# Kernel optimization log

Measured on AMD Instinct MI355X. Metric: run time of the kernel, lower is better.

The kernel has to match this reference:

```python
import jax, jax.numpy as jnp
import numpy as np

N = 50000
E = 1600000
IN_F = 256
OUT_F = 128
ALPHA = 0.2  # LeakyReLU negative slope


def setup_inputs() -> dict:
    key = jax.random.key(0)
    k1, k2, k3, k4, k5, k6 = jax.random.split(key, 6)
    h = jax.random.normal(k1, (N, IN_F), dtype=jnp.float32)
    src = jax.random.randint(k2, (E,), 0, N, dtype=jnp.int64)
    dst = jax.random.randint(k3, (E,), 0, N, dtype=jnp.int64)
    # xavier_uniform-style init
    def xavier(k, shape):
        bound = np.sqrt(6.0 / (shape[0] + shape[1]))
        return jax.random.uniform(k, shape, jnp.float32, -bound, bound)
    W = xavier(k4, (IN_F, OUT_F))
    a_src = xavier(k5, (OUT_F, 1))
    a_dst = xavier(k6, (OUT_F, 1))
    return {"h": h, "src": src, "dst": dst, "W": W, "a_src": a_src, "a_dst": a_dst}


def reference(h, src, dst, W, a_src, a_dst):
    n = h.shape[0]
    Wh = h @ W                                  # [N, OUT_F] dense GEMM
    f1 = (Wh @ a_src)[:, 0]                     # [N]
    f2 = (Wh @ a_dst)[:, 0]                     # [N]
    e = f1[src] + f2[dst]                       # [E] edge-wise gather
    e = jnp.where(e > 0, e, ALPHA * e)          # LeakyReLU
    # sparse softmax over each row (segment = src/row index)
    m = jax.ops.segment_max(e, src, num_segments=n)
    ex = jnp.exp(e - m[src])
    denom = jax.ops.segment_sum(ex, src, num_segments=n)
    att = ex / denom[src]                       # [E] normalized attention
    # sparse-dense matmul: h_prime[i] = sum_j att[ij] * Wh[j]
    h_prime = jax.ops.segment_sum(att[:, None] * Wh[dst], src, num_segments=n)
    return jax.nn.elu(h_prime)
```

## Files before the change

kernel.cpp:

```cpp
#include <hip/hip_runtime.h>
#include <hip/hip_bf16.h>
#include <math.h>

#define IN_F 256
#define OUT_F 128
#define ALPHA 0.2f

#define BSH 7
#define BNODES 128
#define CHUNK 8192
#define NBK 512
#define CAP 5120

typedef __attribute__((ext_vector_type(8))) short short8;
typedef __attribute__((ext_vector_type(4))) float f32x4;

static __device__ __forceinline__ unsigned short f2bf(float x) {
    union { __hip_bfloat16 h; unsigned short u; } cv;
    cv.h = __float2bfloat16(x);
    return cv.u;
}

static __device__ __forceinline__ float2 bf2u(unsigned int u) {
    union { float f; unsigned int i; } a, b;
    a.i = u << 16;
    b.i = u & 0xFFFF0000u;
    return make_float2(a.f, b.f);
}

__global__ __launch_bounds__(512) void scatter_gemm_kernel(
        const int* __restrict__ src, const int* __restrict__ dst,
        int* __restrict__ cursor, unsigned int* __restrict__ bin, int e, int nb,
        const float* __restrict__ h, const float* __restrict__ W,
        const float* __restrict__ a_src, const float* __restrict__ a_dst,
        unsigned short* __restrict__ Whb, float* __restrict__ f1,
        float* __restrict__ f2, int n, int nsc) {
    __shared__ union {
        struct {
            unsigned int ebuf[CHUNK];
            int lh[NBK];
            int ls[NBK];
            int ebase[NBK];
            int lx[NBK];
            int gbase[NBK];
        } sc;
        struct {
            unsigned short a[128 * 40];
            unsigned short b[128 * 40];
        } ge;
    } sm;
    int tid = threadIdx.x;

    if ((int)blockIdx.x < nsc) {
        int base = blockIdx.x * CHUNK;
        int count = e - base; if (count > CHUNK) count = CHUNK;

        for (int i = tid; i < nb; i += 512) sm.sc.lh[i] = 0;
        __syncthreads();
        for (int i = tid; i < count; i += 512) atomicAdd(&sm.sc.lh[src[base + i] >> BSH], 1);
        __syncthreads();
        int v = (tid < nb) ? sm.sc.lh[tid] : 0;
        sm.sc.ls[tid] = v;
        __syncthreads();
#pragma unroll
        for (int off = 1; off < NBK; off <<= 1) {
            int t = (tid >= off) ? sm.sc.ls[tid - off] : 0;
            __syncthreads();
            sm.sc.ls[tid] += t;
            __syncthreads();
        }
        if (tid < nb) {
            int ex = sm.sc.ls[tid] - v;
            sm.sc.ebase[tid] = ex;
            sm.sc.lx[tid] = ex;
        }
        __syncthreads();
        for (int i = tid; i < count; i += 512) {
            int s = src[base + i], d = dst[base + i];
            int b = s >> BSH;
            int p = atomicAdd(&sm.sc.lx[b], 1);
            sm.sc.ebuf[p] = ((unsigned int)(s & (BNODES - 1)) << 17) | (unsigned int)d;
        }
        __syncthreads();
        if (tid < nb) {
            int c = sm.sc.lh[tid];
            sm.sc.gbase[tid] = c ? atomicAdd(&cursor[tid], c) : 0;
        }
        __syncthreads();
        int wave = tid >> 6, lane = tid & 63;
        for (int b = wave; b < nb; b += 8) {
            int c = sm.sc.lh[b], eb = sm.sc.ebase[b], gb = sm.sc.gbase[b];
            size_t gb0 = (size_t)b * CAP + gb;
            for (int l = lane; l < c; l += 64) bin[gb0 + l] = sm.sc.ebuf[eb + l];
        }
    } else {
        int bid = blockIdx.x - nsc;
        int wv = tid >> 6, lane = tid & 63;
        int m = lane & 15, quad = lane >> 4;
        int r0 = bid * 128;

        f32x4 acc[8];
#pragma unroll
        for (int c = 0; c < 8; c++) acc[c] = (f32x4){0.f, 0.f, 0.f, 0.f};

        for (int k0 = 0; k0 < IN_F; k0 += 32) {
            {
                int arow = tid >> 3;
                int kq = tid & 7;
#pragma unroll
                for (int p = 0; p < 2; p++) {
                    int row = arow + p * 64;
                    int grow = r0 + row;
                    float4 v = make_float4(0.f, 0.f, 0.f, 0.f);
                    if (grow < n) v = *(const float4*)&h[(size_t)grow * IN_F + k0 + kq * 4];
                    ushort4 b;
                    b.x = f2bf(v.x); b.y = f2bf(v.y); b.z = f2bf(v.z); b.w = f2bf(v.w);
                    *(ushort4*)&sm.ge.a[row * 40 + kq * 4] = b;
                }
            }
            {
                int c4 = (tid & 31) * 4;
                int kb = tid >> 5;
#pragma unroll
                for (int p = 0; p < 2; p++) {
                    int kk = p * 16 + kb;
                    float4 wv4 = *(const float4*)&W[(size_t)(k0 + kk) * OUT_F + c4];
                    sm.ge.b[(c4 + 0) * 40 + kk] = f2bf(wv4.x);
                    sm.ge.b[(c4 + 1) * 40 + kk] = f2bf(wv4.y);
                    sm.ge.b[(c4 + 2) * 40 + kk] = f2bf(wv4.z);
                    sm.ge.b[(c4 + 3) * 40 + kk] = f2bf(wv4.w);
                }
            }
            __syncthreads();
            short8 af = *(const short8*)&sm.ge.a[(wv * 16 + m) * 40 + quad * 8];
#pragma unroll
            for (int c = 0; c < 8; c++) {
                short8 bfv = *(const short8*)&sm.ge.b[(c * 16 + m) * 40 + quad * 8];
                acc[c] = __builtin_amdgcn_mfma_f32_16x16x32_bf16(af, bfv, acc[c], 0, 0, 0);
            }
            __syncthreads();
        }

        int base_row = r0 + wv * 16 + quad * 4;
#pragma unroll
        for (int reg = 0; reg < 4; reg++) {
            int rg = base_row + reg;
            if (rg < n) {
#pragma unroll
                for (int c = 0; c < 8; c++)
                    Whb[(size_t)rg * OUT_F + c * 16 + m] = f2bf(acc[c][reg]);
            }
        }

        float a1[8], a2[8];
#pragma unroll
        for (int c = 0; c < 8; c++) {
            a1[c] = a_src[c * 16 + m];
            a2[c] = a_dst[c * 16 + m];
        }
        float p1[4] = {0.f, 0.f, 0.f, 0.f}, p2[4] = {0.f, 0.f, 0.f, 0.f};
#pragma unroll
        for (int c = 0; c < 8; c++)
#pragma unroll
            for (int reg = 0; reg < 4; reg++) {
                p1[reg] += acc[c][reg] * a1[c];
                p2[reg] += acc[c][reg] * a2[c];
            }
#pragma unroll
        for (int mask = 1; mask < 16; mask <<= 1)
#pragma unroll
            for (int reg = 0; reg < 4; reg++) {
                p1[reg] += __shfl_xor(p1[reg], mask, 64);
                p2[reg] += __shfl_xor(p2[reg], mask, 64);
            }
        if (m == 0) {
#pragma unroll
            for (int reg = 0; reg < 4; reg++) {
                int rg = base_row + reg;
                if (rg < n) { f1[rg] = p1[reg]; f2[rg] = p2[reg]; }
            }
        }
    }
}

__global__ __launch_bounds__(256) void sort_kernel(const int* __restrict__ cursor,
                                                   const unsigned int* __restrict__ bin,
                                                   uint2* __restrict__ edat,
                                                   int* __restrict__ offs,
                                                   int* __restrict__ deg,
                                                   const float* __restrict__ f1,
                                                   const float* __restrict__ f2, int n) {
    __shared__ unsigned int ebuf[CAP];
    __shared__ int lh[BNODES];
    __shared__ int lx[BNODES];
    __shared__ float lf1[BNODES];
    int b = blockIdx.x;
    int tid = threadIdx.x;
    int base = b * CAP;
    int K = cursor[b];
    if (K > CAP) K = CAP;
    for (int l = tid; l < BNODES; l += 256) {
        lh[l] = 0;
        int node = (b << BSH) + l;
        lf1[l] = (node < n) ? f1[node] : 0.f;
    }
    __syncthreads();
    for (int i = tid; i < K; i += 256) {
        unsigned int p = bin[base + i];
        ebuf[i] = p;
        atomicAdd(&lh[p >> 17], 1);
    }
    __syncthreads();
    int own = (tid < BNODES) ? lh[tid] : 0;
    for (int off = 1; off < BNODES; off <<= 1) {
        int v = (tid >= off && tid < BNODES) ? lh[tid - off] : 0;
        __syncthreads();
        if (tid < BNODES) lh[tid] += v;
        __syncthreads();
    }
    if (tid < BNODES) {
        int ex = lh[tid] - own;
        lx[tid] = ex;
        int node = (b << BSH) + tid;
        if (node < n) { offs[node] = base + ex; deg[node] = own; }
    }
    __syncthreads();
    for (int i = tid; i < K; i += 256) {
        unsigned int p = ebuf[i];
        int ls_ = p >> 17;
        int d = p & 0x1FFFF;
        int r = atomicAdd(&lx[ls_], 1);
        float e = lf1[ls_] + f2[d];
        e = e > 0.f ? e : ALPHA * e;
        edat[base + r] = make_uint2((unsigned int)d, __float_as_uint(__expf(e)));
    }
}

__global__ __launch_bounds__(256) void agg_kernel(const unsigned int* __restrict__ WhbU,
                                                  const int* __restrict__ offs,
                                                  const int* __restrict__ deg,
                                                  const uint2* __restrict__ edat,
                                                  float* __restrict__ out, int n) {
    int tid = threadIdx.x;
    int lane = tid & 63;
    int node = blockIdx.x * 4 + (tid >> 6);
    if (node >= n) return;
    int grp = lane >> 4;
    int c8 = lane & 15;
    int j0 = offs[node];
    int j1 = j0 + deg[node];
    float4 accA = make_float4(0.f, 0.f, 0.f, 0.f);
    float4 accB = make_float4(0.f, 0.f, 0.f, 0.f);
    float den = 0.f;

    int j = j0;
    int nmain = (j1 - j0) >> 4;
    if (nmain > 0) {
        uint2 e0 = edat[j + grp];
        uint2 e1 = edat[j + grp + 4];
        uint2 e2 = edat[j + grp + 8];
        uint2 e3 = edat[j + grp + 12];
        for (int it = 0; it < nmain; ++it) {
            uint4 w0 = *(const uint4*)&WhbU[(size_t)(e0.x << 6) + c8 * 4];
            uint4 w1 = *(const uint4*)&WhbU[(size_t)(e1.x << 6) + c8 * 4];
            uint4 w2 = *(const uint4*)&WhbU[(size_t)(e2.x << 6) + c8 * 4];
            uint4 w3 = *(const uint4*)&WhbU[(size_t)(e3.x << 6) + c8 * 4];
            float x0 = __uint_as_float(e0.y);
            float x1 = __uint_as_float(e1.y);
            float x2 = __uint_as_float(e2.y);
            float x3 = __uint_as_float(e3.y);
            int jn = j + 16;
            uint2 n0, n1, n2, n3;
            if (it + 1 < nmain) {
                n0 = edat[jn + grp];
                n1 = edat[jn + grp + 4];
                n2 = edat[jn + grp + 8];
                n3 = edat[jn + grp + 12];
            }
            float2 g;
            g = bf2u(w0.x); accA.x += x0 * g.x; accA.y += x0 * g.y;
            g = bf2u(w0.y); accA.z += x0 * g.x; accA.w += x0 * g.y;
            g = bf2u(w0.z); accB.x += x0 * g.x; accB.y += x0 * g.y;
            g = bf2u(w0.w); accB.z += x0 * g.x; accB.w += x0 * g.y;
            g = bf2u(w1.x); accA.x += x1 * g.x; accA.y += x1 * g.y;
            g = bf2u(w1.y); accA.z += x1 * g.x; accA.w += x1 * g.y;
            g = bf2u(w1.z); accB.x += x1 * g.x; accB.y += x1 * g.y;
            g = bf2u(w1.w); accB.z += x1 * g.x; accB.w += x1 * g.y;
            g = bf2u(w2.x); accA.x += x2 * g.x; accA.y += x2 * g.y;
            g = bf2u(w2.y); accA.z += x2 * g.x; accA.w += x2 * g.y;
            g = bf2u(w2.z); accB.x += x2 * g.x; accB.y += x2 * g.y;
            g = bf2u(w2.w); accB.z += x2 * g.x; accB.w += x2 * g.y;
            g = bf2u(w3.x); accA.x += x3 * g.x; accA.y += x3 * g.y;
            g = bf2u(w3.y); accA.z += x3 * g.x; accA.w += x3 * g.y;
            g = bf2u(w3.z); accB.x += x3 * g.x; accB.y += x3 * g.y;
            g = bf2u(w3.w); accB.z += x3 * g.x; accB.w += x3 * g.y;
            den += x0 + x1 + x2 + x3;
            j = jn;
            e0 = n0; e1 = n1; e2 = n2; e3 = n3;
        }
    }
    for (; j + 4 <= j1; j += 4) {
        uint2 e = edat[j + grp];
        uint4 w = *(const uint4*)&WhbU[(size_t)(e.x << 6) + c8 * 4];
        float x = __uint_as_float(e.y);
        float2 g;
        g = bf2u(w.x); accA.x += x * g.x; accA.y += x * g.y;
        g = bf2u(w.y); accA.z += x * g.x; accA.w += x * g.y;
        g = bf2u(w.z); accB.x += x * g.x; accB.y += x * g.y;
        g = bf2u(w.w); accB.z += x * g.x; accB.w += x * g.y;
        den += x;
    }
    if (j + grp < j1) {
        uint2 e = edat[j + grp];
        uint4 w = *(const uint4*)&WhbU[(size_t)(e.x << 6) + c8 * 4];
        float x = __uint_as_float(e.y);
        float2 g;
        g = bf2u(w.x); accA.x += x * g.x; accA.y += x * g.y;
        g = bf2u(w.y); accA.z += x * g.x; accA.w += x * g.y;
        g = bf2u(w.z); accB.x += x * g.x; accB.y += x * g.y;
        g = bf2u(w.w); accB.z += x * g.x; accB.w += x * g.y;
        den += x;
    }

#pragma unroll
    for (int mask = 16; mask < 64; mask <<= 1) {
        accA.x += __shfl_xor(accA.x, mask, 64);
        accA.y += __shfl_xor(accA.y, mask, 64);
        accA.z += __shfl_xor(accA.z, mask, 64);
        accA.w += __shfl_xor(accA.w, mask, 64);
        accB.x += __shfl_xor(accB.x, mask, 64);
        accB.y += __shfl_xor(accB.y, mask, 64);
        accB.z += __shfl_xor(accB.z, mask, 64);
        accB.w += __shfl_xor(accB.w, mask, 64);
        den += __shfl_xor(den, mask, 64);
    }

    if (grp == 0) {
        float inv = (j1 > j0) ? 1.f / den : 0.f;
        float r[8];
        r[0] = accA.x * inv; r[1] = accA.y * inv; r[2] = accA.z * inv; r[3] = accA.w * inv;
        r[4] = accB.x * inv; r[5] = accB.y * inv; r[6] = accB.z * inv; r[7] = accB.w * inv;
#pragma unroll
        for (int k = 0; k < 8; k++) r[k] = r[k] > 0.f ? r[k] : __expf(r[k]) - 1.f;
        float* op = &out[(size_t)node * OUT_F + c8 * 8];
        *(float4*)&op[0] = make_float4(r[0], r[1], r[2], r[3]);
        *(float4*)&op[4] = make_float4(r[4], r[5], r[6], r[7]);
    }
}

extern "C" void kernel_launch(void* const* d_in, const int* in_sizes, int n_in,
                              void* d_out, int out_size, void* d_ws, size_t ws_size,
                              hipStream_t stream) {
    const float* h     = (const float*)d_in[0];
    const int*   src   = (const int*)d_in[1];
    const int*   dst   = (const int*)d_in[2];
    const float* W     = (const float*)d_in[3];
    const float* a_src = (const float*)d_in[4];
    const float* a_dst = (const float*)d_in[5];
    float* out = (float*)d_out;

    const int N = in_sizes[0] / IN_F;
    const int E = in_sizes[1];
    const int NB = (N + BNODES - 1) >> BSH;
    const int NCH = (E + CHUNK - 1) / CHUNK;
    const int GB = (N + 127) / 128;

    char* ws = (char*)d_ws;
    size_t off = 0;
    auto alloc = [&](size_t bytes) -> void* {
        void* p = ws + off;
        off += (bytes + 255) & ~(size_t)255;
        return p;
    };
    unsigned short* Whb = (unsigned short*)alloc((size_t)N * OUT_F * 2);
    float* f1     = (float*)alloc((size_t)N * 4);
    float* f2     = (float*)alloc((size_t)N * 4);
    int*   cursor = (int*)alloc((size_t)NB * 4);
    int*   offs   = (int*)alloc((size_t)N * 4);
    int*   deg    = (int*)alloc((size_t)N * 4);
    unsigned int* bin  = (unsigned int*)alloc((size_t)NB * CAP * 4);
    uint2*        edat = (uint2*)alloc((size_t)NB * CAP * 8);
    (void)ws_size; (void)n_in; (void)out_size;

    hipMemsetAsync(cursor, 0, (size_t)NB * 4, stream);
    scatter_gemm_kernel<<<NCH + GB, 512, 0, stream>>>(src, dst, cursor, bin, E, NB,
                                                      h, W, a_src, a_dst, Whb, f1, f2, N, NCH);
    sort_kernel<<<NB, 256, 0, stream>>>(cursor, bin, edat, offs, deg, f1, f2, N);
    agg_kernel<<<(N + 3) / 4, 256, 0, stream>>>((const unsigned int*)Whb, offs, deg, edat, out, N);
}
```

Measured before the change: 211.6 us.

## Fuse bucket sort and aggregation into one kernel using LDS edge list

Merges the sort and aggregation kernels so each block sorts its 128-node bucket into shared memory and immediately aggregates from it. This drops the global edat/offs/deg round trip and one launch, and replaces the barrier-heavy LDS scan with a wave shuffle scan. The W tile load is also reorganized to pack 8 bf16 values per thread into one vector LDS store, and the accumulation uses packed float2 math. The trade-off is fewer blocks (one per 128 nodes, about 391) with large LDS use, which lowers occupancy and latency hiding for the gather-heavy aggregation. The explicit prefetch of the next edge group is also gone.

```diff
diff --git a/kernel.cpp b/kernel.cpp
--- a/kernel.cpp
+++ b/kernel.cpp
@@ -14,6 +14,7 @@
 
 typedef __attribute__((ext_vector_type(8))) short short8;
 typedef __attribute__((ext_vector_type(4))) float f32x4;
+typedef __attribute__((ext_vector_type(2))) float f32x2;
 
 static __device__ __forceinline__ unsigned short f2bf(float x) {
     union { __hip_bfloat16 h; unsigned short u; } cv;
@@ -21,11 +22,11 @@
     return cv.u;
 }
 
-static __device__ __forceinline__ float2 bf2u(unsigned int u) {
-    union { float f; unsigned int i; } a, b;
-    a.i = u << 16;
-    b.i = u & 0xFFFF0000u;
-    return make_float2(a.f, b.f);
+static __device__ __forceinline__ f32x2 up2(unsigned int u) {
+    union { float f; unsigned int i; } lo, hi;
+    lo.i = u << 16;
+    hi.i = u & 0xFFFF0000u;
+    return (f32x2){lo.f, hi.f};
 }
 
 __global__ __launch_bounds__(512) void scatter_gemm_kernel(
@@ -103,6 +104,9 @@
 #pragma unroll
         for (int c = 0; c < 8; c++) acc[c] = (f32x4){0.f, 0.f, 0.f, 0.f};
 
+        int bcol = tid & 127;
+        int bkq  = tid >> 7;
+
         for (int k0 = 0; k0 < IN_F; k0 += 32) {
             {
                 int arow = tid >> 3;
@@ -119,17 +123,14 @@
                 }
             }
             {
-                int c4 = (tid & 31) * 4;
-                int kb = tid >> 5;
-#pragma unroll
-                for (int p = 0; p < 2; p++) {
-                    int kk = p * 16 + kb;
-                    float4 wv4 = *(const float4*)&W[(size_t)(k0 + kk) * OUT_F + c4];
-                    sm.ge.b[(c4 + 0) * 40 + kk] = f2bf(wv4.x);
-                    sm.ge.b[(c4 + 1) * 40 + kk] = f2bf(wv4.y);
-                    sm.ge.b[(c4 + 2) * 40 + kk] = f2bf(wv4.z);
-                    sm.ge.b[(c4 + 3) * 40 + kk] = f2bf(wv4.w);
-                }
+                float vw[8];
+#pragma unroll
+                for (int j = 0; j < 8; ++j)
+                    vw[j] = W[(size_t)(k0 + bkq * 8 + j) * OUT_F + bcol];
+                union { short8 v; unsigned short u[8]; } pk;
+#pragma unroll
+                for (int j = 0; j < 8; ++j) pk.u[j] = f2bf(vw[j]);
+                *(short8*)&sm.ge.b[bcol * 40 + bkq * 8] = pk.v;
             }
             __syncthreads();
             short8 af = *(const short8*)&sm.ge.a[(wv * 16 + m) * 40 + quad * 8];
@@ -183,168 +184,150 @@
     }
 }
 
-__global__ __launch_bounds__(256) void sort_kernel(const int* __restrict__ cursor,
-                                                   const unsigned int* __restrict__ bin,
-                                                   uint2* __restrict__ edat,
-                                                   int* __restrict__ offs,
-                                                   int* __restrict__ deg,
-                                                   const float* __restrict__ f1,
-                                                   const float* __restrict__ f2, int n) {
-    __shared__ unsigned int ebuf[CAP];
+__global__ __launch_bounds__(512) void sortagg_kernel(
+        const int* __restrict__ cursor, const unsigned int* __restrict__ bin,
+        const float* __restrict__ f1, const float* __restrict__ f2,
+        const unsigned int* __restrict__ WhbU, float* __restrict__ out, int n) {
+    __shared__ uint2 eL[CAP];
     __shared__ int lh[BNODES];
-    __shared__ int lx[BNODES];
+    __shared__ int st[BNODES];
+    __shared__ int cur[BNODES];
+    __shared__ int scn[BNODES];
     __shared__ float lf1[BNODES];
     int b = blockIdx.x;
     int tid = threadIdx.x;
     int base = b * CAP;
     int K = cursor[b];
     if (K > CAP) K = CAP;
-    for (int l = tid; l < BNODES; l += 256) {
-        lh[l] = 0;
+
+    if (tid < BNODES) {
+        lh[tid] = 0;
+        int node = (b << BSH) + tid;
+        lf1[tid] = (node < n) ? f1[node] : 0.f;
+    }
+    __syncthreads();
+
+    unsigned int pe[10];
+#pragma unroll
+    for (int u = 0; u < 10; ++u) {
+        int i = tid + u * 512;
+        if (i < K) {
+            unsigned int p = bin[base + i];
+            pe[u] = p;
+            atomicAdd(&lh[p >> 17], 1);
+        }
+    }
+    __syncthreads();
+
+    if (tid < BNODES) {
+        int lane = tid & 63;
+        int s = lh[tid];
+#pragma unroll
+        for (int off = 1; off < 64; off <<= 1) {
+            int t = __shfl_up(s, off, 64);
+            if (lane >= off) s += t;
+        }
+        scn[tid] = s;
+    }
+    __syncthreads();
+    if (tid < BNODES) {
+        int inc = scn[tid] + ((tid >= 64) ? scn[63] : 0);
+        int start = inc - lh[tid];
+        st[tid] = start;
+        cur[tid] = start;
+    }
+    __syncthreads();
+
+#pragma unroll
+    for (int u = 0; u < 10; ++u) {
+        int i = tid + u * 512;
+        if (i < K) {
+            unsigned int p = pe[u];
+            int ls_ = p >> 17;
+            int d = p & 0x1FFFF;
+            int r = atomicAdd(&cur[ls_], 1);
+            float e = lf1[ls_] + f2[d];
+            e = e > 0.f ? e : ALPHA * e;
+            eL[r] = make_uint2((unsigned int)d, __float_as_uint(__expf(e)));
+        }
+    }
+    __syncthreads();
+
+    int wv = tid >> 6, lane = tid & 63;
+    int grp = lane >> 4, c8 = lane & 15;
+    for (int li = 0; li < 16; ++li) {
+        int l = (wv << 4) + li;
         int node = (b << BSH) + l;
-        lf1[l] = (node < n) ? f1[node] : 0.f;
-    }
-    __syncthreads();
-    for (int i = tid; i < K; i += 256) {
-        unsigned int p = bin[base + i];
-        ebuf[i] = p;
-        atomicAdd(&lh[p >> 17], 1);
-    }
-    __syncthreads();
-    int own = (tid < BNODES) ? lh[tid] : 0;
-    for (int off = 1; off < BNODES; off <<= 1) {
-        int v = (tid >= off && tid < BNODES) ? lh[tid - off] : 0;
-        __syncthreads();
-        if (tid < BNODES) lh[tid] += v;
-        __syncthreads();
-    }
-    if (tid < BNODES) {
-        int ex = lh[tid] - own;
-        lx[tid] = ex;
-        int node = (b << BSH) + tid;
-        if (node < n) { offs[node] = base + ex; deg[node] = own; }
-    }
-    __syncthreads();
-    for (int i = tid; i < K; i += 256) {
-        unsigned int p = ebuf[i];
-        int ls_ = p >> 17;
-        int d = p & 0x1FFFF;
-        int r = atomicAdd(&lx[ls_], 1);
-        float e = lf1[ls_] + f2[d];
-        e = e > 0.f ? e : ALPHA * e;
-        edat[base + r] = make_uint2((unsigned int)d, __float_as_uint(__expf(e)));
-    }
-}
-
-__global__ __launch_bounds__(256) void agg_kernel(const unsigned int* __restrict__ WhbU,
-                                                  const int* __restrict__ offs,
-                                                  const int* __restrict__ deg,
-                                                  const uint2* __restrict__ edat,
-                                                  float* __restrict__ out, int n) {
-    int tid = threadIdx.x;
-    int lane = tid & 63;
-    int node = blockIdx.x * 4 + (tid >> 6);
-    if (node >= n) return;
-    int grp = lane >> 4;
-    int c8 = lane & 15;
-    int j0 = offs[node];
-    int j1 = j0 + deg[node];
-    float4 accA = make_float4(0.f, 0.f, 0.f, 0.f);
-    float4 accB = make_float4(0.f, 0.f, 0.f, 0.f);
-    float den = 0.f;
-
-    int j = j0;
-    int nmain = (j1 - j0) >> 4;
-    if (nmain > 0) {
-        uint2 e0 = edat[j + grp];
-        uint2 e1 = edat[j + grp + 4];
-        uint2 e2 = edat[j + grp + 8];
-        uint2 e3 = edat[j + grp + 12];
-        for (int it = 0; it < nmain; ++it) {
-            uint4 w0 = *(const uint4*)&WhbU[(size_t)(e0.x << 6) + c8 * 4];
-            uint4 w1 = *(const uint4*)&WhbU[(size_t)(e1.x << 6) + c8 * 4];
-            uint4 w2 = *(const uint4*)&WhbU[(size_t)(e2.x << 6) + c8 * 4];
-            uint4 w3 = *(const uint4*)&WhbU[(size_t)(e3.x << 6) + c8 * 4];
+        int dg = lh[l];
+        int j = st[l];
+        int jend = j + dg;
+        f32x2 a0 = {0.f, 0.f}, a1 = {0.f, 0.f}, a2 = {0.f, 0.f}, a3 = {0.f, 0.f};
+        float den = 0.f;
+        for (; j + 16 <= jend; j += 16) {
+            uint2 e0 = eL[j + grp];
+            uint2 e1 = eL[j + grp + 4];
+            uint2 e2 = eL[j + grp + 8];
+            uint2 e3 = eL[j + grp + 12];
+            uint4 w0 = *(const uint4*)&WhbU[((size_t)e0.x << 6) + (c8 << 2)];
+            uint4 w1 = *(const uint4*)&WhbU[((size_t)e1.x << 6) + (c8 << 2)];
+            uint4 w2 = *(const uint4*)&WhbU[((size_t)e2.x << 6) + (c8 << 2)];
+            uint4 w3 = *(const uint4*)&WhbU[((size_t)e3.x << 6) + (c8 << 2)];
             float x0 = __uint_as_float(e0.y);
             float x1 = __uint_as_float(e1.y);
             float x2 = __uint_as_float(e2.y);
             float x3 = __uint_as_float(e3.y);
-            int jn = j + 16;
-            uint2 n0, n1, n2, n3;
-            if (it + 1 < nmain) {
-                n0 = edat[jn + grp];
-                n1 = edat[jn + grp + 4];
-                n2 = edat[jn + grp + 8];
-                n3 = edat[jn + grp + 12];
-            }
-            float2 g;
-            g = bf2u(w0.x); accA.x += x0 * g.x; accA.y += x0 * g.y;
-            g = bf2u(w0.y); accA.z += x0 * g.x; accA.w += x0 * g.y;
-            g = bf2u(w0.z); accB.x += x0 * g.x; accB.y += x0 * g.y;
-            g = bf2u(w0.w); accB.z += x0 * g.x; accB.w += x0 * g.y;
-            g = bf2u(w1.x); accA.x += x1 * g.x; accA.y += x1 * g.y;
-            g = bf2u(w1.y); accA.z += x1 * g.x; accA.w += x1 * g.y;
-            g = bf2u(w1.z); accB.x += x1 * g.x; accB.y += x1 * g.y;
-            g = bf2u(w1.w); accB.z += x1 * g.x; accB.w += x1 * g.y;
-            g = bf2u(w2.x); accA.x += x2 * g.x; accA.y += x2 * g.y;
-            g = bf2u(w2.y); accA.z += x2 * g.x; accA.w += x2 * g.y;
-            g = bf2u(w2.z); accB.x += x2 * g.x; accB.y += x2 * g.y;
-            g = bf2u(w2.w); accB.z += x2 * g.x; accB.w += x2 * g.y;
-            g = bf2u(w3.x); accA.x += x3 * g.x; accA.y += x3 * g.y;
-            g = bf2u(w3.y); accA.z += x3 * g.x; accA.w += x3 * g.y;
-            g = bf2u(w3.z); accB.x += x3 * g.x; accB.y += x3 * g.y;
-            g = bf2u(w3.w); accB.z += x3 * g.x; accB.w += x3 * g.y;
+            f32x2 xx;
+            xx = (f32x2){x0, x0};
+            a0 += xx * up2(w0.x); a1 += xx * up2(w0.y); a2 += xx * up2(w0.z); a3 += xx * up2(w0.w);
+            xx = (f32x2){x1, x1};
+            a0 += xx * up2(w1.x); a1 += xx * up2(w1.y); a2 += xx * up2(w1.z); a3 += xx * up2(w1.w);
+            xx = (f32x2){x2, x2};
+            a0 += xx * up2(w2.x); a1 += xx * up2(w2.y); a2 += xx * up2(w2.z); a3 += xx * up2(w2.w);
+            xx = (f32x2){x3, x3};
+            a0 += xx * up2(w3.x); a1 += xx * up2(w3.y); a2 += xx * up2(w3.z); a3 += xx * up2(w3.w);
             den += x0 + x1 + x2 + x3;
-            j = jn;
-            e0 = n0; e1 = n1; e2 = n2; e3 = n3;
-        }
-    }
-    for (; j + 4 <= j1; j += 4) {
-        uint2 e = edat[j + grp];
-        uint4 w = *(const uint4*)&WhbU[(size_t)(e.x << 6) + c8 * 4];
-        float x = __uint_as_float(e.y);
-        float2 g;
-        g = bf2u(w.x); accA.x += x * g.x; accA.y += x * g.y;
-        g = bf2u(w.y); accA.z += x * g.x; accA.w += x * g.y;
-        g = bf2u(w.z); accB.x += x * g.x; accB.y += x * g.y;
-        g = bf2u(w.w); accB.z += x * g.x; accB.w += x * g.y;
-        den += x;
-    }
-    if (j + grp < j1) {
-        uint2 e = edat[j + grp];
-        uint4 w = *(const uint4*)&WhbU[(size_t)(e.x << 6) + c8 * 4];
-        float x = __uint_as_float(e.y);
-        float2 g;
-        g = bf2u(w.x); accA.x += x * g.x; accA.y += x * g.y;
-        g = bf2u(w.y); accA.z += x * g.x; accA.w += x * g.y;
-        g = bf2u(w.z); accB.x += x * g.x; accB.y += x * g.y;
-        g = bf2u(w.w); accB.z += x * g.x; accB.w += x * g.y;
-        den += x;
-    }
-
-#pragma unroll
-    for (int mask = 16; mask < 64; mask <<= 1) {
-        accA.x += __shfl_xor(accA.x, mask, 64);
-        accA.y += __shfl_xor(accA.y, mask, 64);
-        accA.z += __shfl_xor(accA.z, mask, 64);
-        accA.w += __shfl_xor(accA.w, mask, 64);
-        accB.x += __shfl_xor(accB.x, mask, 64);
-        accB.y += __shfl_xor(accB.y, mask, 64);
-        accB.z += __shfl_xor(accB.z, mask, 64);
-        accB.w += __shfl_xor(accB.w, mask, 64);
-        den += __shfl_xor(den, mask, 64);
-    }
-
-    if (grp == 0) {
-        float inv = (j1 > j0) ? 1.f / den : 0.f;
-        float r[8];
-        r[0] = accA.x * inv; r[1] = accA.y * inv; r[2] = accA.z * inv; r[3] = accA.w * inv;
-        r[4] = accB.x * inv; r[5] = accB.y * inv; r[6] = accB.z * inv; r[7] = accB.w * inv;
-#pragma unroll
-        for (int k = 0; k < 8; k++) r[k] = r[k] > 0.f ? r[k] : __expf(r[k]) - 1.f;
-        float* op = &out[(size_t)node * OUT_F + c8 * 8];
-        *(float4*)&op[0] = make_float4(r[0], r[1], r[2], r[3]);
-        *(float4*)&op[4] = make_float4(r[4], r[5], r[6], r[7]);
+        }
+        for (; j + 4 <= jend; j += 4) {
+            uint2 e = eL[j + grp];
+            uint4 w = *(const uint4*)&WhbU[((size_t)e.x << 6) + (c8 << 2)];
+            float x = __uint_as_float(e.y);
+            f32x2 xx = {x, x};
+            a0 += xx * up2(w.x); a1 += xx * up2(w.y); a2 += xx * up2(w.z); a3 += xx * up2(w.w);
+            den += x;
+        }
+        if (j + grp < jend) {
+            uint2 e = eL[j + grp];
+            uint4 w = *(const uint4*)&WhbU[((size_t)e.x << 6) + (c8 << 2)];
+            float x = __uint_as_float(e.y);
+            f32x2 xx = {x, x};
+            a0 += xx * up2(w.x); a1 += xx * up2(w.y); a2 += xx * up2(w.z); a3 += xx * up2(w.w);
+            den += x;
+        }
+
+#pragma unroll
+        for (int mask = 16; mask < 64; mask <<= 1) {
+            a0.x += __shfl_xor(a0.x, mask, 64);
+            a0.y += __shfl_xor(a0.y, mask, 64);
+            a1.x += __shfl_xor(a1.x, mask, 64);
+            a1.y += __shfl_xor(a1.y, mask, 64);
+            a2.x += __shfl_xor(a2.x, mask, 64);
+            a2.y += __shfl_xor(a2.y, mask, 64);
+            a3.x += __shfl_xor(a3.x, mask, 64);
+            a3.y += __shfl_xor(a3.y, mask, 64);
+            den += __shfl_xor(den, mask, 64);
+        }
+
+        if (grp == 0 && node < n) {
+            float inv = dg ? 1.f / den : 0.f;
+            float r[8];
+            r[0] = a0.x * inv; r[1] = a0.y * inv; r[2] = a1.x * inv; r[3] = a1.y * inv;
+            r[4] = a2.x * inv; r[5] = a2.y * inv; r[6] = a3.x * inv; r[7] = a3.y * inv;
+#pragma unroll
+            for (int k = 0; k < 8; k++) r[k] = r[k] > 0.f ? r[k] : __expf(r[k]) - 1.f;
+            float* op = &out[(size_t)node * OUT_F + c8 * 8];
+            *(float4*)&op[0] = make_float4(r[0], r[1], r[2], r[3]);
+            *(float4*)&op[4] = make_float4(r[4], r[5], r[6], r[7]);
+        }
     }
 }
 
@@ -376,15 +359,12 @@
     float* f1     = (float*)alloc((size_t)N * 4);
     float* f2     = (float*)alloc((size_t)N * 4);
     int*   cursor = (int*)alloc((size_t)NB * 4);
-    int*   offs   = (int*)alloc((size_t)N * 4);
-    int*   deg    = (int*)alloc((size_t)N * 4);
-    unsigned int* bin  = (unsigned int*)alloc((size_t)NB * CAP * 4);
-    uint2*        edat = (uint2*)alloc((size_t)NB * CAP * 8);
+    unsigned int* bin = (unsigned int*)alloc((size_t)NB * CAP * 4);
     (void)ws_size; (void)n_in; (void)out_size;
 
     hipMemsetAsync(cursor, 0, (size_t)NB * 4, stream);
     scatter_gemm_kernel<<<NCH + GB, 512, 0, stream>>>(src, dst, cursor, bin, E, NB,
                                                       h, W, a_src, a_dst, Whb, f1, f2, N, NCH);
-    sort_kernel<<<NB, 256, 0, stream>>>(cursor, bin, edat, offs, deg, f1, f2, N);
-    agg_kernel<<<(N + 3) / 4, 256, 0, stream>>>((const unsigned int*)Whb, offs, deg, edat, out, N);
-}
+    sortagg_kernel<<<NB, 512, 0, stream>>>(cursor, bin, f1, f2,
+                                           (const unsigned int*)Whb, out, N);
+}
```

After: 189.5 us. -10.5%, faster.
